# Performance work log

Hardware: AMD Instinct MI355X
Metric: run time of the kernel (lower is better)

The kernel has to match this reference:

```python
import jax, jax.numpy as jnp
import numpy as np

N1, N2, B, D = 16000, 16000, 4096, 256


def setup_inputs() -> dict:
    key = jax.random.key(0)
    ks = jax.random.split(key, 11)
    inp = {
        "x1": jax.random.normal(ks[0], (N1, D), dtype=jnp.float32),
        "x_name1": jax.random.normal(ks[1], (N1, D), dtype=jnp.float32),
        "onehot1": jax.random.normal(ks[2], (N1, D), dtype=jnp.float32),
        "x2": jax.random.normal(ks[3], (N2, D), dtype=jnp.float32),
        "x_name2": jax.random.normal(ks[4], (N2, D), dtype=jnp.float32),
        "onehot2": jax.random.normal(ks[5], (N2, D), dtype=jnp.float32),
        # mk MLP params: Linear(D, D//2) -> ReLU -> Linear(D//2, 1) -> Sigmoid
        "W1": jax.random.normal(ks[6], (D, D // 2), dtype=jnp.float32) * 0.05,
        "b1": jnp.zeros((D // 2,), dtype=jnp.float32),
        "W2": jax.random.normal(ks[7], (D // 2, 1), dtype=jnp.float32) * 0.05,
        "b2": jnp.zeros((1,), dtype=jnp.float32),
        "data_batch": jnp.stack(
            [
                jax.random.randint(ks[8], (B,), 0, N1),
                jax.random.randint(ks[9], (B,), 0, N2),
            ],
            axis=1,
        ).astype(jnp.int64),
    }
    return inp


def _mk(h, W1, b1, W2, b2):
    # tiny 2-layer MLP gate with sigmoid output, h: [B, D] -> [B, 1]
    return jax.nn.sigmoid(jax.nn.relu(h @ W1 + b1) @ W2 + b2)


def _side(Xg, Xfull, W1, b1, W2, b2):
    # Xg: [3, B, D] gathered channels; Xfull: [3, N, D] full tables of the OTHER side
    # cross-attention: softmax(Xg @ Xfull^T) @ Xfull + residual
    A = jax.nn.softmax(jnp.einsum("cbd,cnd->cbn", Xg, Xfull), axis=-1)  # [3,B,N]
    Re = jnp.einsum("cbn,cnd->cbd", A, Xfull) + Xg  # [3,B,D]
    kg = jax.nn.softmax(
        jnp.concatenate(
            [_mk(Re[0], W1, b1, W2, b2), _mk(Re[1], W1, b1, W2, b2), _mk(Re[2], W1, b1, W2, b2)],
            axis=-1,
        ),
        axis=-1,
    )  # [B,3]
    return kg


def reference(x1, x_name1, onehot1, x2, x_name2, onehot2, W1, b1, W2, b2, data_batch):
    i1 = data_batch[:, 0]
    i2 = data_batch[:, 1]
    X1 = jnp.stack([x1[i1], x_name1[i1], onehot1[i1]])  # [3,B,D]
    X2 = jnp.stack([x2[i2], x_name2[i2], onehot2[i2]])  # [3,B,D]
    X1_full = jnp.stack([x2, x_name2, onehot2])  # [3,N2,D]
    X2_full = jnp.stack([x1, x_name1, onehot1])  # [3,N1,D]
    kg1 = _side(X1, X1_full, W1, b1, W2, b2)  # [B,3]
    kg2 = _side(X2, X2_full, W1, b1, W2, b2)  # [B,3]
    x_name1_out = x_name1.at[i1].set(x_name1[i1] * kg1[:, 1:2])
    onehot1_out = onehot1.at[i1].set(onehot1[i1] * kg1[:, 2:3])
    x_name2_out = x_name2.at[i2].set(x_name2[i2] * kg2[:, 1:2])
    onehot2_out = onehot2.at[i2].set(onehot2[i2] * kg2[:, 2:3])
    return (x1, x_name1_out, onehot1_out, x2, x_name2_out, onehot2_out)
```

## Files before the change

### kernel.cpp

```cpp
#include <hip/hip_runtime.h>
#include <math.h>

typedef _Float16 f16;
typedef _Float16 f16x4 __attribute__((ext_vector_type(4)));
typedef _Float16 f16x8 __attribute__((ext_vector_type(8)));
typedef float    f32x4 __attribute__((ext_vector_type(4)));

#define N_ROWS 16000
#define DIM    256
#define BATCH  4096
#define TK     64
#define NTILE  250
#define TPS    125
#define KPAD   264
#define VPAD   72

__global__ __launch_bounds__(256) void k_pack(
    const float* __restrict__ m0, const float* __restrict__ m1, const float* __restrict__ m2,
    const float* __restrict__ m3, const float* __restrict__ m4, const float* __restrict__ m5,
    f16* __restrict__ Kbf, f16* __restrict__ Vt)
{
  __shared__ f16 lt[64][VPAD];
  const float* mats[6] = {m0, m1, m2, m3, m4, m5};
  int bid = blockIdx.x;
  int db  = bid & 3;
  int tn  = (bid >> 2) % NTILE;
  int me  = bid / (NTILE * 4);
  const float* src = mats[me];
  int tid = threadIdx.x;
#pragma unroll
  for (int i = 0; i < 4; ++i) {
    int cidx = i * 256 + tid;
    int r = cidx >> 4, cc = (cidx & 15) * 4;
    float4 f = *(const float4*)(src + (size_t)(tn * 64 + r) * DIM + db * 64 + cc);
    f16x4 h = {(f16)f.x, (f16)f.y, (f16)f.z, (f16)f.w};
    *(f16x4*)&lt[r][cc] = h;
    *(f16x4*)(Kbf + (size_t)me * N_ROWS * DIM + (size_t)(tn * 64 + r) * DIM + db * 64 + cc) = h;
  }
  __syncthreads();
#pragma unroll
  for (int i = 0; i < 4; ++i) {
    int cidx = i * 256 + tid;
    int dl = cidx >> 4, nc4 = (cidx & 15) * 4;
    f16x4 hv = { lt[nc4 + 0][dl], lt[nc4 + 1][dl], lt[nc4 + 2][dl], lt[nc4 + 3][dl] };
    *(f16x4*)(Vt + ((size_t)(me * NTILE + tn) * DIM + db * 64 + dl) * TK + nc4) = hv;
  }
}

__global__ __launch_bounds__(256) void k_gather(
    const float* __restrict__ m0, const float* __restrict__ m1, const float* __restrict__ m2,
    const float* __restrict__ m3, const float* __restrict__ m4, const float* __restrict__ m5,
    const int* __restrict__ batch, f16* __restrict__ Qg)
{
  const float* mats[6] = {m0, m1, m2, m3, m4, m5};
  int gid  = blockIdx.x * 4 + (threadIdx.x >> 6);
  int lane = threadIdx.x & 63;
  int s   = gid / (3 * BATCH);
  int rem = gid - s * 3 * BATCH;
  int c   = rem / BATCH;
  int b   = rem - c * BATCH;
  int idx = batch[(size_t)b * 2 + s];
  const float* src = mats[(s == 0 ? 0 : 3) + c] + (size_t)idx * DIM;
  float4 f = *(const float4*)(src + lane * 4);
  f16x4 h = {(f16)f.x, (f16)f.y, (f16)f.z, (f16)f.w};
  *(f16x4*)(Qg + (size_t)gid * DIM + lane * 4) = h;
}

__global__ __launch_bounds__(256, 2) void k_attn(
    const f16* __restrict__ Kbf, const f16* __restrict__ Vt,
    const f16* __restrict__ Qg, f16* __restrict__ Onorm, float* __restrict__ ml)
{
  __shared__ f16 shK[TK][KPAD];
  __shared__ f16 shV[DIM][VPAD];
  __shared__ f16 shP[4][16][VPAD];

  const int bid = blockIdx.x;
  const int v  = bid & 1;
  const int t  = (bid >> 1) & 63;
  const int cs = bid >> 7;
  const int s  = cs / 3, c = cs - s * 3;
  const int kvmat = (s == 0) ? (3 + c) : c;

  const int tid  = threadIdx.x;
  const int lane = tid & 63;
  const int w    = tid >> 6;
  const int l15  = lane & 15;
  const int quad = lane >> 4;

  const f16* Qrow = Qg + ((size_t)cs * BATCH + (size_t)t * 64 + w * 16 + l15) * DIM + quad * 8;
  f16x8 qf[8];
#pragma unroll
  for (int kt = 0; kt < 8; ++kt) qf[kt] = *(const f16x8*)(Qrow + kt * 32);

  f32x4 O[16];
#pragma unroll
  for (int i = 0; i < 16; ++i) O[i] = (f32x4){0.f, 0.f, 0.f, 0.f};
  float m_r[4] = {-INFINITY, -INFINITY, -INFINITY, -INFINITY};
  float l_r[4] = {0.f, 0.f, 0.f, 0.f};

  const uint4* gK0 = (const uint4*)(Kbf + (size_t)kvmat * N_ROWS * DIM);
  const uint4* gV0 = (const uint4*)(Vt + (size_t)kvmat * NTILE * DIM * TK);

  for (int tile = v * TPS; tile < v * TPS + TPS; ++tile) {
    {
      const uint4* gK = gK0 + (size_t)tile * 2048;
      const uint4* gV = gV0 + (size_t)tile * 2048;
      uint4 st[8];
#pragma unroll
      for (int i = 0; i < 8; ++i) st[i] = gK[i * 256 + tid];
#pragma unroll
      for (int i = 0; i < 8; ++i) {
        int ch = i * 256 + tid;
        *(uint4*)&shK[ch >> 5][(ch & 31) * 8] = st[i];
      }
#pragma unroll
      for (int i = 0; i < 8; ++i) st[i] = gV[i * 256 + tid];
#pragma unroll
      for (int i = 0; i < 8; ++i) {
        int ch = i * 256 + tid;
        *(uint4*)&shV[ch >> 3][(ch & 7) * 8] = st[i];
      }
    }
    __syncthreads();

    f32x4 sacc[4];
#pragma unroll
    for (int nc = 0; nc < 4; ++nc) sacc[nc] = (f32x4){0.f, 0.f, 0.f, 0.f};
#pragma unroll
    for (int kt = 0; kt < 8; ++kt) {
#pragma unroll
      for (int nc = 0; nc < 4; ++nc) {
        f16x8 kf = *(const f16x8*)&shK[nc * 16 + l15][kt * 32 + quad * 8];
        sacc[nc] = __builtin_amdgcn_mfma_f32_16x16x32_f16(qf[kt], kf, sacc[nc], 0, 0, 0);
      }
    }

    float alpha[4];
    bool upd = false;
#pragma unroll
    for (int r = 0; r < 4; ++r) {
      float mx = fmaxf(fmaxf(sacc[0][r], sacc[1][r]), fmaxf(sacc[2][r], sacc[3][r]));
#pragma unroll
      for (int off = 1; off < 16; off <<= 1) mx = fmaxf(mx, __shfl_xor(mx, off, 64));
      float mnew = fmaxf(m_r[r], mx);
      alpha[r] = __expf(m_r[r] - mnew);
      upd = upd || (mnew > m_r[r]);
      m_r[r] = mnew;
    }
    float rowsum[4] = {0.f, 0.f, 0.f, 0.f};
#pragma unroll
    for (int nc = 0; nc < 4; ++nc) {
#pragma unroll
      for (int r = 0; r < 4; ++r) {
        float p = __expf(sacc[nc][r] - m_r[r]);
        rowsum[r] += p;
        shP[w][quad * 4 + r][nc * 16 + l15] = (f16)p;
      }
    }
#pragma unroll
    for (int r = 0; r < 4; ++r) {
#pragma unroll
      for (int off = 1; off < 16; off <<= 1) rowsum[r] += __shfl_xor(rowsum[r], off, 64);
      l_r[r] = l_r[r] * alpha[r] + rowsum[r];
    }
    if (__any(upd)) {
#pragma unroll
      for (int nc = 0; nc < 16; ++nc) {
#pragma unroll
        for (int r = 0; r < 4; ++r) O[nc][r] *= alpha[r];
      }
    }

    f16x8 pf0 = *(const f16x8*)&shP[w][l15][quad * 8];
    f16x8 pf1 = *(const f16x8*)&shP[w][l15][32 + quad * 8];
#pragma unroll
    for (int nc = 0; nc < 16; ++nc) {
      f16x8 vf0 = *(const f16x8*)&shV[nc * 16 + l15][quad * 8];
      O[nc] = __builtin_amdgcn_mfma_f32_16x16x32_f16(pf0, vf0, O[nc], 0, 0, 0);
      f16x8 vf1 = *(const f16x8*)&shV[nc * 16 + l15][32 + quad * 8];
      O[nc] = __builtin_amdgcn_mfma_f32_16x16x32_f16(pf1, vf1, O[nc], 0, 0, 0);
    }
    __syncthreads();
  }

  const size_t orow0 = (size_t)(v * 6 + cs) * BATCH + (size_t)t * 64 + w * 16;
  if (l15 == 0) {
#pragma unroll
    for (int r = 0; r < 4; ++r) {
      size_t row = orow0 + quad * 4 + r;
      ml[row * 2 + 0] = m_r[r];
      ml[row * 2 + 1] = l_r[r];
    }
  }
#pragma unroll
  for (int r = 0; r < 4; ++r) {
    float inv = 1.0f / l_r[r];
    size_t row = orow0 + quad * 4 + r;
#pragma unroll
    for (int nc = 0; nc < 16; ++nc)
      Onorm[row * DIM + nc * 16 + l15] = (f16)(O[nc][r] * inv);
  }
}

__global__ __launch_bounds__(256, 2) void k_combine(
    const float* __restrict__ W1, const float* __restrict__ b1,
    const float* __restrict__ W2, const float* __restrict__ b2,
    const f16* __restrict__ Qg, const f16* __restrict__ Onorm,
    const float* __restrict__ ml, float* __restrict__ mval)
{
  __shared__ f16 w1s[DIM * 128];
  __shared__ float reb[4][DIM];
  __shared__ float w2s[128];
  __shared__ float b1s[128];
  int tid = threadIdx.x;
#pragma unroll
  for (int i = 0; i < 32; ++i) {
    int e = i * 1024 + tid * 4;
    float4 f = *(const float4*)(W1 + e);
    f16x4 h = {(f16)f.x, (f16)f.y, (f16)f.z, (f16)f.w};
    *(f16x4*)&w1s[e] = h;
  }
  if (tid < 128) { w2s[tid] = W2[tid]; b1s[tid] = b1[tid]; }
  float b2v = b2[0];
  __syncthreads();

  int w = tid >> 6, lane = tid & 63;
  for (int rr = 0; rr < 8; ++rr) {
    int grow = blockIdx.x * 32 + w * 8 + rr;
    float m0 = ml[grow * 2],            l0 = ml[grow * 2 + 1];
    float m1 = ml[(24576 + grow) * 2],  l1 = ml[(24576 + grow) * 2 + 1];
    float M  = fmaxf(m0, m1);
    float w0  = l0 * __expf(m0 - M);
    float w1v = l1 * __expf(m1 - M);
    float inv = 1.f / (w0 + w1v);
    w0 *= inv; w1v *= inv;
    f16x4 o0 = *(const f16x4*)(Onorm + (size_t)grow * DIM + lane * 4);
    f16x4 o1 = *(const f16x4*)(Onorm + (size_t)(24576 + grow) * DIM + lane * 4);
    f16x4 qv = *(const f16x4*)(Qg + (size_t)grow * DIM + lane * 4);
#pragma unroll
    for (int k = 0; k < 4; ++k)
      reb[w][lane * 4 + k] = w0 * (float)o0[k] + w1v * (float)o1[k] + (float)qv[k];
    float acc0 = b1s[lane], acc1 = b1s[lane + 64];
    for (int d = 0; d < DIM; ++d) {
      float rv = reb[w][d];
      acc0 += rv * (float)w1s[d * 128 + lane];
      acc1 += rv * (float)w1s[d * 128 + 64 + lane];
    }
    float part = fmaxf(acc0, 0.f) * w2s[lane] + fmaxf(acc1, 0.f) * w2s[lane + 64];
#pragma unroll
    for (int off = 1; off < 64; off <<= 1) part += __shfl_xor(part, off, 64);
    if (lane == 0) mval[grow] = 1.f / (1.f + __expf(-(part + b2v)));
  }
}

__global__ __launch_bounds__(256) void k_copy(
    const float* __restrict__ m0, const float* __restrict__ m1, const float* __restrict__ m2,
    const float* __restrict__ m3, const float* __restrict__ m4, const float* __restrict__ m5,
    float* __restrict__ out)
{
  const float* mats[6] = {m0, m1, m2, m3, m4, m5};
  int arr = blockIdx.x / 4000;
  int chunk = (blockIdx.x - arr * 4000) * 256 + threadIdx.x;
  float4 v = *(const float4*)(mats[arr] + (size_t)chunk * 4);
  *(float4*)(out + (size_t)arr * 4096000 + (size_t)chunk * 4) = v;
}

__global__ __launch_bounds__(256) void k_scatter(
    const float* __restrict__ m0, const float* __restrict__ m1, const float* __restrict__ m2,
    const float* __restrict__ m3, const float* __restrict__ m4, const float* __restrict__ m5,
    const int* __restrict__ batch, const float* __restrict__ mval,
    float* __restrict__ out)
{
  const float* mats[6] = {m0, m1, m2, m3, m4, m5};
  int gid  = blockIdx.x * 4 + (threadIdx.x >> 6);
  int lane = threadIdx.x & 63;
  int s = gid >> 12;
  int b = gid & 4095;
  int idx = batch[(size_t)b * 2 + s];
  float v0 = mval[(s * 3 + 0) * BATCH + b];
  float v1 = mval[(s * 3 + 1) * BATCH + b];
  float v2 = mval[(s * 3 + 2) * BATCH + b];
  float mx = fmaxf(v0, fmaxf(v1, v2));
  float e0 = __expf(v0 - mx), e1 = __expf(v1 - mx), e2 = __expf(v2 - mx);
  float inv = 1.f / (e0 + e1 + e2);
  float kgn = e1 * inv;
  float kgo = e2 * inv;
  int a1 = s * 3 + 1, a2 = s * 3 + 2;
  const float* s1 = mats[a1] + (size_t)idx * DIM;
  const float* s2 = mats[a2] + (size_t)idx * DIM;
  float4 f1 = *(const float4*)(s1 + lane * 4);
  float4 f2 = *(const float4*)(s2 + lane * 4);
  float4 r1 = {f1.x * kgn, f1.y * kgn, f1.z * kgn, f1.w * kgn};
  float4 r2 = {f2.x * kgo, f2.y * kgo, f2.z * kgo, f2.w * kgo};
  *(float4*)(out + (size_t)a1 * 4096000 + (size_t)idx * DIM + lane * 4) = r1;
  *(float4*)(out + (size_t)a2 * 4096000 + (size_t)idx * DIM + lane * 4) = r2;
}

extern "C" void kernel_launch(void* const* d_in, const int* in_sizes, int n_in,
                              void* d_out, int out_size, void* d_ws, size_t ws_size,
                              hipStream_t stream)
{
  const float* x1  = (const float*)d_in[0];
  const float* xn1 = (const float*)d_in[1];
  const float* oh1 = (const float*)d_in[2];
  const float* x2  = (const float*)d_in[3];
  const float* xn2 = (const float*)d_in[4];
  const float* oh2 = (const float*)d_in[5];
  const float* W1  = (const float*)d_in[6];
  const float* b1  = (const float*)d_in[7];
  const float* W2  = (const float*)d_in[8];
  const float* b2  = (const float*)d_in[9];
  const int*   batch = (const int*)d_in[10];
  float* out = (float*)d_out;

  f16* Kbf = (f16*)d_out;
  f16* Vt  = (f16*)((char*)d_out + 49152000);

  char* ws = (char*)d_ws;
  f16*   Qg    = (f16*)(ws);
  f16*   Onorm = (f16*)(ws + 12582912);
  float* ml    = (float*)(ws + 37748736);
  float* mval  = (float*)(ws + 38141952);

  k_pack   <<<6000, 256, 0, stream>>>(x1, xn1, oh1, x2, xn2, oh2, Kbf, Vt);
  k_gather <<<6144, 256, 0, stream>>>(x1, xn1, oh1, x2, xn2, oh2, batch, Qg);
  k_attn   <<<768,  256, 0, stream>>>(Kbf, Vt, Qg, Onorm, ml);
  k_combine<<<768,  256, 0, stream>>>(W1, b1, W2, b2, Qg, Onorm, ml, mval);
  k_copy   <<<24000, 256, 0, stream>>>(x1, xn1, oh1, x2, xn2, oh2, out);
  k_scatter<<<2048, 256, 0, stream>>>(x1, xn1, oh1, x2, xn2, oh2, batch, mval, out);
}
```

Baseline: 1.120 ms.

## Double query rows per attention block, XOR-swizzle K/V tiles, load via global_load_lds

Each attention block now handles 128 query rows, two 16-row sets per wave, so every K/V tile staged in LDS feeds twice as many MFMAs. This halves the global K/V traffic and halves the grid to 384 blocks. The pack kernel now writes K and V as contiguous 32KB tile images with an XOR swizzle, so the attention kernel can copy them straight into LDS with global_load_lds. That replaces the register round-trip, and the swizzled reads avoid bank conflicts without padding. The costs are more accumulator registers per wave, which can lower occupancy, and fewer blocks to spread across the CUs.

```diff
diff --git a/kernel.cpp b/kernel.cpp
--- a/kernel.cpp
+++ b/kernel.cpp
@@ -12,15 +12,22 @@
 #define TK     64
 #define NTILE  250
 #define TPS    125
-#define KPAD   264
-#define VPAD   72
+#define QT     128
+#define LTP    72
+
+__device__ __forceinline__ void gload16(const void* g, void* l) {
+  __builtin_amdgcn_global_load_lds(
+      (const __attribute__((address_space(1))) void*)g,
+      (__attribute__((address_space(3))) void*)l, 16, 0, 0);
+}
+
 
 __global__ __launch_bounds__(256) void k_pack(
     const float* __restrict__ m0, const float* __restrict__ m1, const float* __restrict__ m2,
     const float* __restrict__ m3, const float* __restrict__ m4, const float* __restrict__ m5,
-    f16* __restrict__ Kbf, f16* __restrict__ Vt)
-{
-  __shared__ f16 lt[64][VPAD];
+    unsigned char* __restrict__ Kimg, unsigned char* __restrict__ Vimg)
+{
+  __shared__ f16 lt[64][LTP];
   const float* mats[6] = {m0, m1, m2, m3, m4, m5};
   int bid = blockIdx.x;
   int db  = bid & 3;
@@ -28,6 +35,8 @@
   int me  = bid / (NTILE * 4);
   const float* src = mats[me];
   int tid = threadIdx.x;
+  unsigned char* Kt = Kimg + ((size_t)(me * NTILE + tn) << 15);
+  unsigned char* Vt = Vimg + ((size_t)(me * NTILE + tn) << 15);
 #pragma unroll
   for (int i = 0; i < 4; ++i) {
     int cidx = i * 256 + tid;
@@ -35,7 +44,7 @@
     float4 f = *(const float4*)(src + (size_t)(tn * 64 + r) * DIM + db * 64 + cc);
     f16x4 h = {(f16)f.x, (f16)f.y, (f16)f.z, (f16)f.w};
     *(f16x4*)&lt[r][cc] = h;
-    *(f16x4*)(Kbf + (size_t)me * N_ROWS * DIM + (size_t)(tn * 64 + r) * DIM + db * 64 + cc) = h;
+    *(f16x4*)(Kt + r * 512 + ((db * 128 + cc * 2) ^ ((r & 7) << 4))) = h;
   }
   __syncthreads();
 #pragma unroll
@@ -43,7 +52,8 @@
     int cidx = i * 256 + tid;
     int dl = cidx >> 4, nc4 = (cidx & 15) * 4;
     f16x4 hv = { lt[nc4 + 0][dl], lt[nc4 + 1][dl], lt[nc4 + 2][dl], lt[nc4 + 3][dl] };
-    *(f16x4*)(Vt + ((size_t)(me * NTILE + tn) * DIM + db * 64 + dl) * TK + nc4) = hv;
+    int d = db * 64 + dl;
+    *(f16x4*)(Vt + d * 128 + ((nc4 * 2) ^ ((dl & 7) << 4))) = hv;
   }
 }
 
@@ -67,17 +77,17 @@
 }
 
 __global__ __launch_bounds__(256, 2) void k_attn(
-    const f16* __restrict__ Kbf, const f16* __restrict__ Vt,
+    const unsigned char* __restrict__ Kimg, const unsigned char* __restrict__ Vimg,
     const f16* __restrict__ Qg, f16* __restrict__ Onorm, float* __restrict__ ml)
 {
-  __shared__ f16 shK[TK][KPAD];
-  __shared__ f16 shV[DIM][VPAD];
-  __shared__ f16 shP[4][16][VPAD];
+  __shared__ unsigned char shK[32768];
+  __shared__ unsigned char shV[32768];
+  __shared__ unsigned char shP[4][4096];
 
   const int bid = blockIdx.x;
   const int v  = bid & 1;
-  const int t  = (bid >> 1) & 63;
-  const int cs = bid >> 7;
+  const int t  = (bid >> 1) & 31;
+  const int cs = bid >> 6;
   const int s  = cs / 3, c = cs - s * 3;
   const int kvmat = (s == 0) ? (3 + c) : c;
 
@@ -86,119 +96,131 @@
   const int w    = tid >> 6;
   const int l15  = lane & 15;
   const int quad = lane >> 4;
-
-  const f16* Qrow = Qg + ((size_t)cs * BATCH + (size_t)t * 64 + w * 16 + l15) * DIM + quad * 8;
-  f16x8 qf[8];
-#pragma unroll
-  for (int kt = 0; kt < 8; ++kt) qf[kt] = *(const f16x8*)(Qrow + kt * 32);
-
-  f32x4 O[16];
-#pragma unroll
-  for (int i = 0; i < 16; ++i) O[i] = (f32x4){0.f, 0.f, 0.f, 0.f};
-  float m_r[4] = {-INFINITY, -INFINITY, -INFINITY, -INFINITY};
-  float l_r[4] = {0.f, 0.f, 0.f, 0.f};
-
-  const uint4* gK0 = (const uint4*)(Kbf + (size_t)kvmat * N_ROWS * DIM);
-  const uint4* gV0 = (const uint4*)(Vt + (size_t)kvmat * NTILE * DIM * TK);
+  const int xr   = (l15 & 7) << 4;
+  unsigned char* shPw = shP[w];
+
+  const f16* Qrow = Qg + ((size_t)cs * BATCH + (size_t)t * QT + w * 32 + l15) * DIM + quad * 8;
+  f16x8 qf[2][8];
+#pragma unroll
+  for (int a = 0; a < 2; ++a)
+#pragma unroll
+    for (int kt = 0; kt < 8; ++kt)
+      qf[a][kt] = *(const f16x8*)(Qrow + a * 16 * DIM + kt * 32);
+
+  f32x4 O[2][16];
+#pragma unroll
+  for (int a = 0; a < 2; ++a)
+#pragma unroll
+    for (int i = 0; i < 16; ++i) O[a][i] = (f32x4){0.f, 0.f, 0.f, 0.f};
+  float m_r[2][4], l_r[2][4];
+#pragma unroll
+  for (int a = 0; a < 2; ++a)
+#pragma unroll
+    for (int r = 0; r < 4; ++r) { m_r[a][r] = -INFINITY; l_r[a][r] = 0.f; }
+
+  const unsigned char* gK0 = Kimg + ((size_t)(kvmat * NTILE) << 15);
+  const unsigned char* gV0 = Vimg + ((size_t)(kvmat * NTILE) << 15);
+  const int o = tid * 16;
 
   for (int tile = v * TPS; tile < v * TPS + TPS; ++tile) {
-    {
-      const uint4* gK = gK0 + (size_t)tile * 2048;
-      const uint4* gV = gV0 + (size_t)tile * 2048;
-      uint4 st[8];
-#pragma unroll
-      for (int i = 0; i < 8; ++i) st[i] = gK[i * 256 + tid];
-#pragma unroll
-      for (int i = 0; i < 8; ++i) {
-        int ch = i * 256 + tid;
-        *(uint4*)&shK[ch >> 5][(ch & 31) * 8] = st[i];
-      }
-#pragma unroll
-      for (int i = 0; i < 8; ++i) st[i] = gV[i * 256 + tid];
-#pragma unroll
-      for (int i = 0; i < 8; ++i) {
-        int ch = i * 256 + tid;
-        *(uint4*)&shV[ch >> 3][(ch & 7) * 8] = st[i];
-      }
-    }
+    const unsigned char* gK = gK0 + ((size_t)tile << 15);
+    const unsigned char* gV = gV0 + ((size_t)tile << 15);
+#pragma unroll
+    for (int i = 0; i < 8; ++i) gload16(gK + i * 4096 + o, shK + i * 4096 + o);
+#pragma unroll
+    for (int i = 0; i < 8; ++i) gload16(gV + i * 4096 + o, shV + i * 4096 + o);
     __syncthreads();
 
-    f32x4 sacc[4];
-#pragma unroll
-    for (int nc = 0; nc < 4; ++nc) sacc[nc] = (f32x4){0.f, 0.f, 0.f, 0.f};
+    f32x4 sacc[2][4];
+#pragma unroll
+    for (int a = 0; a < 2; ++a)
+#pragma unroll
+      for (int nc = 0; nc < 4; ++nc) sacc[a][nc] = (f32x4){0.f, 0.f, 0.f, 0.f};
 #pragma unroll
     for (int kt = 0; kt < 8; ++kt) {
 #pragma unroll
       for (int nc = 0; nc < 4; ++nc) {
-        f16x8 kf = *(const f16x8*)&shK[nc * 16 + l15][kt * 32 + quad * 8];
-        sacc[nc] = __builtin_amdgcn_mfma_f32_16x16x32_f16(qf[kt], kf, sacc[nc], 0, 0, 0);
-      }
-    }
-
-    float alpha[4];
-    bool upd = false;
+        f16x8 kf = *(const f16x8*)(shK + (nc * 16 + l15) * 512 + ((kt * 64 + quad * 16) ^ xr));
+        sacc[0][nc] = __builtin_amdgcn_mfma_f32_16x16x32_f16(qf[0][kt], kf, sacc[0][nc], 0, 0, 0);
+        sacc[1][nc] = __builtin_amdgcn_mfma_f32_16x16x32_f16(qf[1][kt], kf, sacc[1][nc], 0, 0, 0);
+      }
+    }
+
+#pragma unroll
+    for (int a = 0; a < 2; ++a) {
+      float alpha[4]; bool upd = false;
+#pragma unroll
+      for (int r = 0; r < 4; ++r) {
+        float mx = fmaxf(fmaxf(sacc[a][0][r], sacc[a][1][r]), fmaxf(sacc[a][2][r], sacc[a][3][r]));
+#pragma unroll
+        for (int off = 1; off < 16; off <<= 1) mx = fmaxf(mx, __shfl_xor(mx, off, 64));
+        float mnew = fmaxf(m_r[a][r], mx);
+        alpha[r] = __expf(m_r[a][r] - mnew);
+        upd = upd || (mnew > m_r[a][r]);
+        m_r[a][r] = mnew;
+      }
+      float rs[4] = {0.f, 0.f, 0.f, 0.f};
+#pragma unroll
+      for (int nc = 0; nc < 4; ++nc) {
+#pragma unroll
+        for (int r = 0; r < 4; ++r) {
+          float p = __expf(sacc[a][nc][r] - m_r[a][r]);
+          rs[r] += p;
+          const int qr = quad * 4 + r;
+          *(f16*)(shPw + (a * 16 + qr) * 128 + ((nc * 32 + l15 * 2) ^ ((qr & 7) << 4))) = (f16)p;
+        }
+      }
+#pragma unroll
+      for (int r = 0; r < 4; ++r) {
+#pragma unroll
+        for (int off = 1; off < 16; off <<= 1) rs[r] += __shfl_xor(rs[r], off, 64);
+        l_r[a][r] = l_r[a][r] * alpha[r] + rs[r];
+      }
+      if (__any(upd)) {
+#pragma unroll
+        for (int nc = 0; nc < 16; ++nc)
+#pragma unroll
+          for (int r = 0; r < 4; ++r) O[a][nc][r] *= alpha[r];
+      }
+    }
+
+    f16x8 pf[2][2];
+#pragma unroll
+    for (int a = 0; a < 2; ++a)
+#pragma unroll
+      for (int h = 0; h < 2; ++h)
+        pf[a][h] = *(const f16x8*)(shPw + (a * 16 + l15) * 128 + ((h * 64 + quad * 16) ^ xr));
+#pragma unroll
+    for (int nc = 0; nc < 16; ++nc) {
+      f16x8 vf0 = *(const f16x8*)(shV + (nc * 16 + l15) * 128 + ((quad * 16) ^ xr));
+      f16x8 vf1 = *(const f16x8*)(shV + (nc * 16 + l15) * 128 + ((64 + quad * 16) ^ xr));
+      O[0][nc] = __builtin_amdgcn_mfma_f32_16x16x32_f16(pf[0][0], vf0, O[0][nc], 0, 0, 0);
+      O[0][nc] = __builtin_amdgcn_mfma_f32_16x16x32_f16(pf[0][1], vf1, O[0][nc], 0, 0, 0);
+      O[1][nc] = __builtin_amdgcn_mfma_f32_16x16x32_f16(pf[1][0], vf0, O[1][nc], 0, 0, 0);
+      O[1][nc] = __builtin_amdgcn_mfma_f32_16x16x32_f16(pf[1][1], vf1, O[1][nc], 0, 0, 0);
+    }
+    __syncthreads();
+  }
+
+#pragma unroll
+  for (int a = 0; a < 2; ++a) {
+    const size_t orow0 = (size_t)(v * 6 + cs) * BATCH + (size_t)t * QT + w * 32 + a * 16;
+    if (l15 == 0) {
+#pragma unroll
+      for (int r = 0; r < 4; ++r) {
+        size_t row = orow0 + quad * 4 + r;
+        ml[row * 2 + 0] = m_r[a][r];
+        ml[row * 2 + 1] = l_r[a][r];
+      }
+    }
 #pragma unroll
     for (int r = 0; r < 4; ++r) {
-      float mx = fmaxf(fmaxf(sacc[0][r], sacc[1][r]), fmaxf(sacc[2][r], sacc[3][r]));
-#pragma unroll
-      for (int off = 1; off < 16; off <<= 1) mx = fmaxf(mx, __shfl_xor(mx, off, 64));
-      float mnew = fmaxf(m_r[r], mx);
-      alpha[r] = __expf(m_r[r] - mnew);
-      upd = upd || (mnew > m_r[r]);
-      m_r[r] = mnew;
-    }
-    float rowsum[4] = {0.f, 0.f, 0.f, 0.f};
-#pragma unroll
-    for (int nc = 0; nc < 4; ++nc) {
-#pragma unroll
-      for (int r = 0; r < 4; ++r) {
-        float p = __expf(sacc[nc][r] - m_r[r]);
-        rowsum[r] += p;
-        shP[w][quad * 4 + r][nc * 16 + l15] = (f16)p;
-      }
-    }
-#pragma unroll
-    for (int r = 0; r < 4; ++r) {
-#pragma unroll
-      for (int off = 1; off < 16; off <<= 1) rowsum[r] += __shfl_xor(rowsum[r], off, 64);
-      l_r[r] = l_r[r] * alpha[r] + rowsum[r];
-    }
-    if (__any(upd)) {
-#pragma unroll
-      for (int nc = 0; nc < 16; ++nc) {
-#pragma unroll
-        for (int r = 0; r < 4; ++r) O[nc][r] *= alpha[r];
-      }
-    }
-
-    f16x8 pf0 = *(const f16x8*)&shP[w][l15][quad * 8];
-    f16x8 pf1 = *(const f16x8*)&shP[w][l15][32 + quad * 8];
-#pragma unroll
-    for (int nc = 0; nc < 16; ++nc) {
-      f16x8 vf0 = *(const f16x8*)&shV[nc * 16 + l15][quad * 8];
-      O[nc] = __builtin_amdgcn_mfma_f32_16x16x32_f16(pf0, vf0, O[nc], 0, 0, 0);
-      f16x8 vf1 = *(const f16x8*)&shV[nc * 16 + l15][32 + quad * 8];
-      O[nc] = __builtin_amdgcn_mfma_f32_16x16x32_f16(pf1, vf1, O[nc], 0, 0, 0);
-    }
-    __syncthreads();
-  }
-
-  const size_t orow0 = (size_t)(v * 6 + cs) * BATCH + (size_t)t * 64 + w * 16;
-  if (l15 == 0) {
-#pragma unroll
-    for (int r = 0; r < 4; ++r) {
+      float inv = 1.0f / l_r[a][r];
       size_t row = orow0 + quad * 4 + r;
-      ml[row * 2 + 0] = m_r[r];
-      ml[row * 2 + 1] = l_r[r];
-    }
-  }
-#pragma unroll
-  for (int r = 0; r < 4; ++r) {
-    float inv = 1.0f / l_r[r];
-    size_t row = orow0 + quad * 4 + r;
-#pragma unroll
-    for (int nc = 0; nc < 16; ++nc)
-      Onorm[row * DIM + nc * 16 + l15] = (f16)(O[nc][r] * inv);
+#pragma unroll
+      for (int nc = 0; nc < 16; ++nc)
+        Onorm[row * DIM + nc * 16 + l15] = (f16)(O[a][nc][r] * inv);
+    }
   }
 }
 
@@ -313,8 +335,8 @@
   const int*   batch = (const int*)d_in[10];
   float* out = (float*)d_out;
 
-  f16* Kbf = (f16*)d_out;
-  f16* Vt  = (f16*)((char*)d_out + 49152000);
+  unsigned char* Kimg = (unsigned char*)d_out;
+  unsigned char* Vimg = (unsigned char*)d_out + 49152000;
 
   char* ws = (char*)d_ws;
   f16*   Qg    = (f16*)(ws);
@@ -322,9 +344,9 @@
   float* ml    = (float*)(ws + 37748736);
   float* mval  = (float*)(ws + 38141952);
 
-  k_pack   <<<6000, 256, 0, stream>>>(x1, xn1, oh1, x2, xn2, oh2, Kbf, Vt);
+  k_pack   <<<6000, 256, 0, stream>>>(x1, xn1, oh1, x2, xn2, oh2, Kimg, Vimg);
   k_gather <<<6144, 256, 0, stream>>>(x1, xn1, oh1, x2, xn2, oh2, batch, Qg);
-  k_attn   <<<768,  256, 0, stream>>>(Kbf, Vt, Qg, Onorm, ml);
+  k_attn   <<<384,  256, 0, stream>>>(Kimg, Vimg, Qg, Onorm, ml);
   k_combine<<<768,  256, 0, stream>>>(W1, b1, W2, b2, Qg, Onorm, ml, mval);
   k_copy   <<<24000, 256, 0, stream>>>(x1, xn1, oh1, x2, xn2, oh2, out);
   k_scatter<<<2048, 256, 0, stream>>>(x1, xn1, oh1, x2, xn2, oh2, batch, mval, out);
```

Measured after the change: 1.265 ms. 13.0% more time.

## Pre-swizzle K/V tiles in global memory and prefetch next tile into registers

Applied to the files above, without the earlier changes.

The pack kernel now writes K and V as 32KB per-tile images that already carry an XOR swizzle, so the attention kernel copies them into unpadded shared memory with straight 16-byte stores. The MFMA operand reads, including the P buffer, use the matching XOR addressing to avoid LDS bank conflicts without padding. The next tile's global loads are issued into registers before the current tile's compute, overlapping memory latency with MFMA work. s_setprio is raised around the MFMA loops. The cost is 16 uint4 staging registers per thread, which adds register pressure at two blocks per SM.

```diff
diff --git a/kernel.cpp b/kernel.cpp
--- a/kernel.cpp
+++ b/kernel.cpp
@@ -12,15 +12,16 @@
 #define TK     64
 #define NTILE  250
 #define TPS    125
-#define KPAD   264
-#define VPAD   72
+#define QT     64
+#define LTP    72
+
 
 __global__ __launch_bounds__(256) void k_pack(
     const float* __restrict__ m0, const float* __restrict__ m1, const float* __restrict__ m2,
     const float* __restrict__ m3, const float* __restrict__ m4, const float* __restrict__ m5,
-    f16* __restrict__ Kbf, f16* __restrict__ Vt)
-{
-  __shared__ f16 lt[64][VPAD];
+    unsigned char* __restrict__ Kimg, unsigned char* __restrict__ Vimg)
+{
+  __shared__ f16 lt[64][LTP];
   const float* mats[6] = {m0, m1, m2, m3, m4, m5};
   int bid = blockIdx.x;
   int db  = bid & 3;
@@ -28,6 +29,8 @@
   int me  = bid / (NTILE * 4);
   const float* src = mats[me];
   int tid = threadIdx.x;
+  unsigned char* Kt = Kimg + ((size_t)(me * NTILE + tn) << 15);
+  unsigned char* Vt = Vimg + ((size_t)(me * NTILE + tn) << 15);
 #pragma unroll
   for (int i = 0; i < 4; ++i) {
     int cidx = i * 256 + tid;
@@ -35,7 +38,7 @@
     float4 f = *(const float4*)(src + (size_t)(tn * 64 + r) * DIM + db * 64 + cc);
     f16x4 h = {(f16)f.x, (f16)f.y, (f16)f.z, (f16)f.w};
     *(f16x4*)&lt[r][cc] = h;
-    *(f16x4*)(Kbf + (size_t)me * N_ROWS * DIM + (size_t)(tn * 64 + r) * DIM + db * 64 + cc) = h;
+    *(f16x4*)(Kt + r * 512 + ((db * 128 + cc * 2) ^ ((r & 7) << 4))) = h;
   }
   __syncthreads();
 #pragma unroll
@@ -43,7 +46,8 @@
     int cidx = i * 256 + tid;
     int dl = cidx >> 4, nc4 = (cidx & 15) * 4;
     f16x4 hv = { lt[nc4 + 0][dl], lt[nc4 + 1][dl], lt[nc4 + 2][dl], lt[nc4 + 3][dl] };
-    *(f16x4*)(Vt + ((size_t)(me * NTILE + tn) * DIM + db * 64 + dl) * TK + nc4) = hv;
+    int d = db * 64 + dl;
+    *(f16x4*)(Vt + d * 128 + ((nc4 * 2) ^ ((dl & 7) << 4))) = hv;
   }
 }
 
@@ -67,12 +71,12 @@
 }
 
 __global__ __launch_bounds__(256, 2) void k_attn(
-    const f16* __restrict__ Kbf, const f16* __restrict__ Vt,
+    const unsigned char* __restrict__ Kimg, const unsigned char* __restrict__ Vimg,
     const f16* __restrict__ Qg, f16* __restrict__ Onorm, float* __restrict__ ml)
 {
-  __shared__ f16 shK[TK][KPAD];
-  __shared__ f16 shV[DIM][VPAD];
-  __shared__ f16 shP[4][16][VPAD];
+  __shared__ unsigned char shK[32768];
+  __shared__ unsigned char shV[32768];
+  __shared__ unsigned char shP[4][2048];
 
   const int bid = blockIdx.x;
   const int v  = bid & 1;
@@ -86,8 +90,10 @@
   const int w    = tid >> 6;
   const int l15  = lane & 15;
   const int quad = lane >> 4;
-
-  const f16* Qrow = Qg + ((size_t)cs * BATCH + (size_t)t * 64 + w * 16 + l15) * DIM + quad * 8;
+  const int xr   = (l15 & 7) << 4;
+  unsigned char* Pw = shP[w];
+
+  const f16* Qrow = Qg + ((size_t)cs * BATCH + (size_t)t * QT + w * 16 + l15) * DIM + quad * 8;
   f16x8 qf[8];
 #pragma unroll
   for (int kt = 0; kt < 8; ++kt) qf[kt] = *(const f16x8*)(Qrow + kt * 32);
@@ -98,42 +104,51 @@
   float m_r[4] = {-INFINITY, -INFINITY, -INFINITY, -INFINITY};
   float l_r[4] = {0.f, 0.f, 0.f, 0.f};
 
-  const uint4* gK0 = (const uint4*)(Kbf + (size_t)kvmat * N_ROWS * DIM);
-  const uint4* gV0 = (const uint4*)(Vt + (size_t)kvmat * NTILE * DIM * TK);
-
-  for (int tile = v * TPS; tile < v * TPS + TPS; ++tile) {
+  const unsigned char* gK0 = Kimg + ((size_t)(kvmat * NTILE) << 15);
+  const unsigned char* gV0 = Vimg + ((size_t)(kvmat * NTILE) << 15);
+  const int o = tid * 16;
+  const int t0 = v * TPS, t1 = t0 + TPS;
+
+  uint4 st[16];
+  {
+    const uint4* gK = (const uint4*)(gK0 + ((size_t)t0 << 15));
+    const uint4* gV = (const uint4*)(gV0 + ((size_t)t0 << 15));
+#pragma unroll
+    for (int i = 0; i < 8; ++i) st[i]     = gK[i * 256 + tid];
+#pragma unroll
+    for (int i = 0; i < 8; ++i) st[8 + i] = gV[i * 256 + tid];
+  }
+
+  for (int tile = t0; tile < t1; ++tile) {
+#pragma unroll
+    for (int i = 0; i < 8; ++i) *(uint4*)(shK + i * 4096 + o) = st[i];
+#pragma unroll
+    for (int i = 0; i < 8; ++i) *(uint4*)(shV + i * 4096 + o) = st[8 + i];
+    __syncthreads();
+
     {
-      const uint4* gK = gK0 + (size_t)tile * 2048;
-      const uint4* gV = gV0 + (size_t)tile * 2048;
-      uint4 st[8];
-#pragma unroll
-      for (int i = 0; i < 8; ++i) st[i] = gK[i * 256 + tid];
-#pragma unroll
-      for (int i = 0; i < 8; ++i) {
-        int ch = i * 256 + tid;
-        *(uint4*)&shK[ch >> 5][(ch & 31) * 8] = st[i];
-      }
-#pragma unroll
-      for (int i = 0; i < 8; ++i) st[i] = gV[i * 256 + tid];
-#pragma unroll
-      for (int i = 0; i < 8; ++i) {
-        int ch = i * 256 + tid;
-        *(uint4*)&shV[ch >> 3][(ch & 7) * 8] = st[i];
-      }
-    }
-    __syncthreads();
+      int tn = (tile + 1 < t1) ? tile + 1 : tile;
+      const uint4* gK = (const uint4*)(gK0 + ((size_t)tn << 15));
+      const uint4* gV = (const uint4*)(gV0 + ((size_t)tn << 15));
+#pragma unroll
+      for (int i = 0; i < 8; ++i) st[i]     = gK[i * 256 + tid];
+#pragma unroll
+      for (int i = 0; i < 8; ++i) st[8 + i] = gV[i * 256 + tid];
+    }
 
     f32x4 sacc[4];
 #pragma unroll
     for (int nc = 0; nc < 4; ++nc) sacc[nc] = (f32x4){0.f, 0.f, 0.f, 0.f};
+    __builtin_amdgcn_s_setprio(1);
 #pragma unroll
     for (int kt = 0; kt < 8; ++kt) {
 #pragma unroll
       for (int nc = 0; nc < 4; ++nc) {
-        f16x8 kf = *(const f16x8*)&shK[nc * 16 + l15][kt * 32 + quad * 8];
+        f16x8 kf = *(const f16x8*)(shK + (nc * 16 + l15) * 512 + ((kt * 64 + quad * 16) ^ xr));
         sacc[nc] = __builtin_amdgcn_mfma_f32_16x16x32_f16(qf[kt], kf, sacc[nc], 0, 0, 0);
       }
     }
+    __builtin_amdgcn_s_setprio(0);
 
     float alpha[4];
     bool upd = false;
@@ -154,7 +169,8 @@
       for (int r = 0; r < 4; ++r) {
         float p = __expf(sacc[nc][r] - m_r[r]);
         rowsum[r] += p;
-        shP[w][quad * 4 + r][nc * 16 + l15] = (f16)p;
+        int q = quad * 4 + r;
+        *(f16*)(Pw + q * 128 + ((nc * 32 + l15 * 2) ^ ((q & 7) << 4))) = (f16)p;
       }
     }
 #pragma unroll
@@ -171,19 +187,21 @@
       }
     }
 
-    f16x8 pf0 = *(const f16x8*)&shP[w][l15][quad * 8];
-    f16x8 pf1 = *(const f16x8*)&shP[w][l15][32 + quad * 8];
+    f16x8 pf0 = *(const f16x8*)(Pw + l15 * 128 + ((quad * 16) ^ xr));
+    f16x8 pf1 = *(const f16x8*)(Pw + l15 * 128 + ((64 + quad * 16) ^ xr));
+    __builtin_amdgcn_s_setprio(1);
 #pragma unroll
     for (int nc = 0; nc < 16; ++nc) {
-      f16x8 vf0 = *(const f16x8*)&shV[nc * 16 + l15][quad * 8];
+      f16x8 vf0 = *(const f16x8*)(shV + (nc * 16 + l15) * 128 + ((quad * 16) ^ xr));
       O[nc] = __builtin_amdgcn_mfma_f32_16x16x32_f16(pf0, vf0, O[nc], 0, 0, 0);
-      f16x8 vf1 = *(const f16x8*)&shV[nc * 16 + l15][32 + quad * 8];
+      f16x8 vf1 = *(const f16x8*)(shV + (nc * 16 + l15) * 128 + ((64 + quad * 16) ^ xr));
       O[nc] = __builtin_amdgcn_mfma_f32_16x16x32_f16(pf1, vf1, O[nc], 0, 0, 0);
     }
+    __builtin_amdgcn_s_setprio(0);
     __syncthreads();
   }
 
-  const size_t orow0 = (size_t)(v * 6 + cs) * BATCH + (size_t)t * 64 + w * 16;
+  const size_t orow0 = (size_t)(v * 6 + cs) * BATCH + (size_t)t * QT + w * 16;
   if (l15 == 0) {
 #pragma unroll
     for (int r = 0; r < 4; ++r) {
@@ -313,8 +331,8 @@
   const int*   batch = (const int*)d_in[10];
   float* out = (float*)d_out;
 
-  f16* Kbf = (f16*)d_out;
-  f16* Vt  = (f16*)((char*)d_out + 49152000);
+  unsigned char* Kimg = (unsigned char*)d_out;
+  unsigned char* Vimg = (unsigned char*)d_out + 49152000;
 
   char* ws = (char*)d_ws;
   f16*   Qg    = (f16*)(ws);
@@ -322,9 +340,9 @@
   float* ml    = (float*)(ws + 37748736);
   float* mval  = (float*)(ws + 38141952);
 
-  k_pack   <<<6000, 256, 0, stream>>>(x1, xn1, oh1, x2, xn2, oh2, Kbf, Vt);
+  k_pack   <<<6000, 256, 0, stream>>>(x1, xn1, oh1, x2, xn2, oh2, Kimg, Vimg);
   k_gather <<<6144, 256, 0, stream>>>(x1, xn1, oh1, x2, xn2, oh2, batch, Qg);
-  k_attn   <<<768,  256, 0, stream>>>(Kbf, Vt, Qg, Onorm, ml);
+  k_attn   <<<768,  256, 0, stream>>>(Kimg, Vimg, Qg, Onorm, ml);
   k_combine<<<768,  256, 0, stream>>>(W1, b1, W2, b2, Qg, Onorm, ml, mval);
   k_copy   <<<24000, 256, 0, stream>>>(x1, xn1, oh1, x2, xn2, oh2, out);
   k_scatter<<<2048, 256, 0, stream>>>(x1, xn1, oh1, x2, xn2, oh2, batch, mval, out);
```

Result: slower. 2.204 ms (+96.8%).

## Swap MFMA operand order so each lane owns one query row

Applied to the files above, without the earlier changes.

Swaps the A/B operands of both attention MFMAs so the accumulator is transposed: each lane holds four key (or feature) columns of a single query row instead of four rows. The online-softmax max and sum reductions then need two cross-lane shuffles instead of sixteen, rescaling uses one scalar alpha, and P and the output are written as packed f16x4 vectors instead of scalar stores. This cuts shuffle and scalar store overhead in the softmax inner loop, at the cost of a different LDS write pattern for P that may bank-conflict.

```diff
diff --git a/kernel.cpp b/kernel.cpp
--- a/kernel.cpp
+++ b/kernel.cpp
@@ -14,6 +14,7 @@
 #define TPS    125
 #define KPAD   264
 #define VPAD   72
+#define PPAD   72
 
 __global__ __launch_bounds__(256) void k_pack(
     const float* __restrict__ m0, const float* __restrict__ m1, const float* __restrict__ m2,
@@ -72,7 +73,7 @@
 {
   __shared__ f16 shK[TK][KPAD];
   __shared__ f16 shV[DIM][VPAD];
-  __shared__ f16 shP[4][16][VPAD];
+  __shared__ f16 shP[4][16][PPAD];
 
   const int bid = blockIdx.x;
   const int v  = bid & 1;
@@ -95,8 +96,8 @@
   f32x4 O[16];
 #pragma unroll
   for (int i = 0; i < 16; ++i) O[i] = (f32x4){0.f, 0.f, 0.f, 0.f};
-  float m_r[4] = {-INFINITY, -INFINITY, -INFINITY, -INFINITY};
-  float l_r[4] = {0.f, 0.f, 0.f, 0.f};
+  float m_r = -INFINITY;
+  float l_r = 0.f;
 
   const uint4* gK0 = (const uint4*)(Kbf + (size_t)kvmat * N_ROWS * DIM);
   const uint4* gV0 = (const uint4*)(Vt + (size_t)kvmat * NTILE * DIM * TK);
@@ -131,44 +132,41 @@
 #pragma unroll
       for (int nc = 0; nc < 4; ++nc) {
         f16x8 kf = *(const f16x8*)&shK[nc * 16 + l15][kt * 32 + quad * 8];
-        sacc[nc] = __builtin_amdgcn_mfma_f32_16x16x32_f16(qf[kt], kf, sacc[nc], 0, 0, 0);
+        sacc[nc] = __builtin_amdgcn_mfma_f32_16x16x32_f16(kf, qf[kt], sacc[nc], 0, 0, 0);
       }
     }
 
-    float alpha[4];
-    bool upd = false;
-#pragma unroll
-    for (int r = 0; r < 4; ++r) {
-      float mx = fmaxf(fmaxf(sacc[0][r], sacc[1][r]), fmaxf(sacc[2][r], sacc[3][r]));
-#pragma unroll
-      for (int off = 1; off < 16; off <<= 1) mx = fmaxf(mx, __shfl_xor(mx, off, 64));
-      float mnew = fmaxf(m_r[r], mx);
-      alpha[r] = __expf(m_r[r] - mnew);
-      upd = upd || (mnew > m_r[r]);
-      m_r[r] = mnew;
-    }
-    float rowsum[4] = {0.f, 0.f, 0.f, 0.f};
+    float mx = sacc[0][0];
+#pragma unroll
+    for (int nc = 0; nc < 4; ++nc)
+#pragma unroll
+      for (int r = 0; r < 4; ++r) mx = fmaxf(mx, sacc[nc][r]);
+    mx = fmaxf(mx, __shfl_xor(mx, 16, 64));
+    mx = fmaxf(mx, __shfl_xor(mx, 32, 64));
+    float mnew = fmaxf(m_r, mx);
+    float alpha = __expf(m_r - mnew);
+    bool upd = (mnew > m_r);
+    m_r = mnew;
+
+    float rowsum = 0.f;
 #pragma unroll
     for (int nc = 0; nc < 4; ++nc) {
+      f16x4 pk;
 #pragma unroll
       for (int r = 0; r < 4; ++r) {
-        float p = __expf(sacc[nc][r] - m_r[r]);
-        rowsum[r] += p;
-        shP[w][quad * 4 + r][nc * 16 + l15] = (f16)p;
+        float p = __expf(sacc[nc][r] - m_r);
+        rowsum += p;
+        pk[r] = (f16)p;
       }
-    }
-#pragma unroll
-    for (int r = 0; r < 4; ++r) {
-#pragma unroll
-      for (int off = 1; off < 16; off <<= 1) rowsum[r] += __shfl_xor(rowsum[r], off, 64);
-      l_r[r] = l_r[r] * alpha[r] + rowsum[r];
-    }
+      *(f16x4*)&shP[w][l15][nc * 16 + quad * 4] = pk;
+    }
+    rowsum += __shfl_xor(rowsum, 16, 64);
+    rowsum += __shfl_xor(rowsum, 32, 64);
+    l_r = l_r * alpha + rowsum;
+
     if (__any(upd)) {
 #pragma unroll
-      for (int nc = 0; nc < 16; ++nc) {
-#pragma unroll
-        for (int r = 0; r < 4; ++r) O[nc][r] *= alpha[r];
-      }
+      for (int nc = 0; nc < 16; ++nc) O[nc] *= alpha;
     }
 
     f16x8 pf0 = *(const f16x8*)&shP[w][l15][quad * 8];
@@ -176,29 +174,24 @@
 #pragma unroll
     for (int nc = 0; nc < 16; ++nc) {
       f16x8 vf0 = *(const f16x8*)&shV[nc * 16 + l15][quad * 8];
-      O[nc] = __builtin_amdgcn_mfma_f32_16x16x32_f16(pf0, vf0, O[nc], 0, 0, 0);
+      O[nc] = __builtin_amdgcn_mfma_f32_16x16x32_f16(vf0, pf0, O[nc], 0, 0, 0);
       f16x8 vf1 = *(const f16x8*)&shV[nc * 16 + l15][32 + quad * 8];
-      O[nc] = __builtin_amdgcn_mfma_f32_16x16x32_f16(pf1, vf1, O[nc], 0, 0, 0);
+      O[nc] = __builtin_amdgcn_mfma_f32_16x16x32_f16(vf1, pf1, O[nc], 0, 0, 0);
     }
     __syncthreads();
   }
 
-  const size_t orow0 = (size_t)(v * 6 + cs) * BATCH + (size_t)t * 64 + w * 16;
-  if (l15 == 0) {
-#pragma unroll
-    for (int r = 0; r < 4; ++r) {
-      size_t row = orow0 + quad * 4 + r;
-      ml[row * 2 + 0] = m_r[r];
-      ml[row * 2 + 1] = l_r[r];
-    }
-  }
-#pragma unroll
-  for (int r = 0; r < 4; ++r) {
-    float inv = 1.0f / l_r[r];
-    size_t row = orow0 + quad * 4 + r;
-#pragma unroll
-    for (int nc = 0; nc < 16; ++nc)
-      Onorm[row * DIM + nc * 16 + l15] = (f16)(O[nc][r] * inv);
+  const size_t orow = (size_t)(v * 6 + cs) * BATCH + (size_t)t * 64 + w * 16 + l15;
+  if (quad == 0) {
+    ml[orow * 2 + 0] = m_r;
+    ml[orow * 2 + 1] = l_r;
+  }
+  float inv = 1.0f / l_r;
+#pragma unroll
+  for (int nc = 0; nc < 16; ++nc) {
+    f16x4 ov = {(f16)(O[nc][0] * inv), (f16)(O[nc][1] * inv),
+                (f16)(O[nc][2] * inv), (f16)(O[nc][3] * inv)};
+    *(f16x4*)(Onorm + orow * DIM + nc * 16 + quad * 4) = ov;
   }
 }
 
```

After: 983.7 us. 1.14x faster.
